# Kernel optimization log

Measured on AMD Instinct MI355X. Metric: run time of the kernel, lower is better.

Reference implementation:

```python
import jax, jax.numpy as jnp
import numpy as np
import math

EMBED_DIM = 128
SCALE = math.sqrt(EMBED_DIM)


def setup_inputs() -> dict:
    key = jax.random.key(0)
    # x: [B, N, D, L] = [4, 16, 128, 2048]
    x = jax.random.normal(key, (4, 16, 128, 2048), dtype=jnp.float32)
    return {"x": x}


def reference(x):
    # x: [B, N, D, L] -> [B, N, L, D]
    xt = jnp.swapaxes(x, -1, -2)
    # scores: [B, N, L, L] = softmax(x x^T / sqrt(D))
    scores = jnp.einsum("bnld,bnmd->bnlm", xt, xt) / jnp.asarray(SCALE, xt.dtype)
    attn = jax.nn.softmax(scores, axis=-1)
    # weighted values then mean over query positions L -> [B, N, D]
    out = jnp.einsum("bnlm,bnmd->bnld", attn, xt).mean(axis=2)
    return out
```

## Files before the change

kernel.cpp:

```cpp
#include <hip/hip_runtime.h>
#include <hip/hip_fp16.h>

#define H_  64
#define D_  128
#define L_  2048
#define PRE 0.35709578f
#define SLOTS 17

typedef _Float16 half8 __attribute__((ext_vector_type(8)));
typedef float    f32x4 __attribute__((ext_vector_type(4)));

__device__ __forceinline__ float fast_exp2(float x) {
#if __has_builtin(__builtin_amdgcn_exp2f)
    return __builtin_amdgcn_exp2f(x);
#else
    return __builtin_exp2f(x);
#endif
}

__device__ __forceinline__ void gload16(const void* g, void* l) {
    __builtin_amdgcn_global_load_lds(
        (const __attribute__((address_space(1))) void*)g,
        (__attribute__((address_space(3))) void*)l,
        16, 0, 0);
}

__device__ __forceinline__ void stage32k(const char* __restrict__ src,
                                         char* __restrict__ dst,
                                         int wid, int lane) {
#pragma unroll
    for (int jj = 0; jj < 8; ++jj) {
        const unsigned o   = (unsigned)(wid * 8 + jj) * 1024u + (unsigned)lane * 16u;
        const unsigned row = o >> 8;
        const unsigned so  = (o & ~255u) | ((o & 255u) ^ ((row & 7u) << 4));
        gload16(src + so, dst + (size_t)(wid * 8 + jj) * 1024u);
    }
}

__global__ __launch_bounds__(256) void k_transpose(const float* __restrict__ x,
                                                   __half* __restrict__ xt) {
    const int h  = blockIdx.x;
    const int lc = blockIdx.y;
    __shared__ float raw[128][65];
    const float* xh = x + (size_t)h * D_ * L_ + (size_t)lc * 64;
    const int t = threadIdx.x;
    const int r0 = t >> 4;
    const int c4 = (t & 15) << 2;
#pragma unroll
    for (int i = 0; i < 8; ++i) {
        const int d = i * 16 + r0;
        const float4 v = *(const float4*)(xh + (size_t)d * L_ + c4);
        raw[d][c4 + 0] = v.x; raw[d][c4 + 1] = v.y;
        raw[d][c4 + 2] = v.z; raw[d][c4 + 3] = v.w;
    }
    __syncthreads();
    const int lane = t & 63, w = t >> 6;
    __half2* xth = (__half2*)(xt + (size_t)h * L_ * D_ + (size_t)lc * 64 * D_);
#pragma unroll
    for (int i = 0; i < 16; ++i) {
        const int jl = w * 16 + i;
        const float a = raw[2 * lane][jl] * PRE;
        const float b = raw[2 * lane + 1][jl] * PRE;
        xth[(size_t)jl * 64 + lane] = __floats2half2_rn(a, b);
    }
}

template <int PASS>
__global__ __launch_bounds__(256, 2) void k_gemm(const __half* __restrict__ xt,
                                                 const float* __restrict__ ainv,
                                                 float* __restrict__ zw) {
    __shared__ char  sm[65536];
    __shared__ float aS[2048];
    __shared__ float csum[2][2][128];
    __shared__ float zfin[2][128];

    const int bid = blockIdx.x;
    const int res = bid & 7;
    const int j   = bid >> 3;
    const int h   = ((j >> 3) << 3) | res;
    const int pid = j & 7;

    const int t    = threadIdx.x;
    const int lane = t & 63;
    const int wid  = t >> 6;
    const int wr   = wid >> 1;
    const int wc   = wid & 1;
    const int lo   = lane & 15, hi = lane >> 4;
    const unsigned sx   = (unsigned)((lane & 7) << 4);
    const unsigned rowA = (unsigned)(wr * 64 + lo);
    const unsigned rowB = (unsigned)(wc * 64 + lo);

    const char* xh  = (const char*)(xt + (size_t)h * (L_ * D_));
    float*      zwh = zw + (size_t)h * SLOTS * 2048;

    if (PASS == 2) {
        const float4* a4 = (const float4*)(ainv + ((size_t)h << 11));
        *(float4*)&aS[t * 8]     = a4[t * 2];
        *(float4*)&aS[t * 8 + 4] = a4[t * 2 + 1];
    }

#pragma unroll 1
    for (int pp = 0; pp < 2; ++pp) {
        const int p  = pp ? (15 - pid) : pid;
        const int NS = 15 - p;

        stage32k(xh + (size_t)p * 32768, sm, wid, lane);
        if (NS > 0) stage32k(xh + (size_t)(p + 1) * 32768, sm + 32768, wid, lane);
        __syncthreads();

        half8 afr[4][4];
#pragma unroll
        for (int fm = 0; fm < 4; ++fm)
#pragma unroll
            for (int s = 0; s < 4; ++s)
                afr[fm][s] = *(const half8*)(sm + (rowA + fm * 16) * 256
                                                + (((unsigned)(s * 64 + hi * 16)) ^ sx));
        float rs[4][4] = {};
        float ar[4][4];
        if (PASS == 2) {
#pragma unroll
            for (int fm = 0; fm < 4; ++fm)
#pragma unroll
                for (int r = 0; r < 4; ++r)
                    ar[fm][r] = aS[p * 128 + wr * 64 + fm * 16 + hi * 4 + r];
        }

#pragma unroll 1
        for (int it = 0; it <= NS; ++it) {
            const int ct = p + it;
            if (it > 0) __syncthreads();
            if (it < NS)
                stage32k(xh + (size_t)(ct + 1) * 32768,
                         sm + (((it + 1) & 1) ? 32768 : 0), wid, lane);
            if (it >= 1 && t < 128) {
                const int pr = (it - 1) & 1;
                const float v = csum[pr][0][t] + csum[pr][1][t];
                if (it == 1) { if (PASS == 2) zwh[((size_t)16 << 11) + (size_t)p * 128 + t] = v; }
                else         zwh[((size_t)p << 11) + (size_t)(ct - 1) * 128 + t] = v;
            }

            const char* bbuf = (it == 0) ? sm : (sm + ((it & 1) ? 32768 : 0));

#pragma unroll 1
            for (int hf = 0; hf < 2; ++hf) {
                float acol[2];
                if (PASS == 2) {
#pragma unroll
                    for (int f = 0; f < 2; ++f)
                        acol[f] = aS[ct * 128 + wc * 64 + (hf * 2 + f) * 16 + lo];
                }
                f32x4 acc[4][2] = {};
                __builtin_amdgcn_s_setprio(1);
#pragma unroll
                for (int s = 0; s < 4; ++s) {
                    const unsigned inr = ((unsigned)(s * 64 + hi * 16)) ^ sx;
                    half8 b[2];
#pragma unroll
                    for (int f = 0; f < 2; ++f)
                        b[f] = *(const half8*)(bbuf + (rowB + (unsigned)(hf * 2 + f) * 16) * 256 + inr);
#pragma unroll
                    for (int fm = 0; fm < 4; ++fm)
#pragma unroll
                        for (int fn = 0; fn < 2; ++fn)
                            acc[fm][fn] = __builtin_amdgcn_mfma_f32_16x16x32_f16(
                                afr[fm][s], b[fn], acc[fm][fn], 0, 0, 0);
                }
                __builtin_amdgcn_s_setprio(0);

                float cs[2] = {0.f, 0.f};
#pragma unroll
                for (int fm = 0; fm < 4; ++fm)
#pragma unroll
                    for (int fn = 0; fn < 2; ++fn)
#pragma unroll
                        for (int r = 0; r < 4; ++r) {
                            const float e = fast_exp2(acc[fm][fn][r]);
                            if (PASS == 1) { rs[fm][r] += e; cs[fn] += e; }
                            else           { cs[fn] += ar[fm][r] * e;
                                             if (it > 0) rs[fm][r] += acol[fn] * e; }
                        }
                if (!(PASS == 1 && it == 0)) {
#pragma unroll
                    for (int fn = 0; fn < 2; ++fn) {
                        cs[fn] += __shfl_xor(cs[fn], 16, 64);
                        cs[fn] += __shfl_xor(cs[fn], 32, 64);
                    }
                    if (lane < 16) {
#pragma unroll
                        for (int fn = 0; fn < 2; ++fn)
                            csum[it & 1][wr][wc * 64 + (hf * 2 + fn) * 16 + lane] = cs[fn];
                    }
                }
            }
        }

#pragma unroll
        for (int fm = 0; fm < 4; ++fm)
#pragma unroll
            for (int r = 0; r < 4; ++r) {
                float v = rs[fm][r];
                v += __shfl_xor(v, 1, 64);
                v += __shfl_xor(v, 2, 64);
                v += __shfl_xor(v, 4, 64);
                v += __shfl_xor(v, 8, 64);
                if (lo == 0) zfin[wc][wr * 64 + fm * 16 + hi * 4 + r] = v;
            }
        __syncthreads();
        if (t < 128) {
            zwh[((size_t)15 << 11) + ((size_t)p << 7) + t] = zfin[0][t] + zfin[1][t];
            const int pr = NS & 1;
            const float v = csum[pr][0][t] + csum[pr][1][t];
            if (NS == 0) { if (PASS == 2) zwh[((size_t)16 << 11) + (size_t)p * 128 + t] = v; }
            else         zwh[((size_t)p << 11) + (size_t)(p + NS) * 128 + t] = v;
        }
    }
}

__global__ __launch_bounds__(256) void k_reduceZ(const float* __restrict__ zp,
                                                 float* __restrict__ ainv) {
    const int i = blockIdx.x * 256 + threadIdx.x;
    const int h = i >> 11, l = i & 2047, q = l >> 7;
    const float* zh = zp + (size_t)h * SLOTS * 2048;
    float z = zh[((size_t)15 << 11) + l];
#pragma unroll
    for (int p = 0; p < 15; ++p)
        if (p < q) z += zh[((size_t)p << 11) + l];
    ainv[i] = 1.0f / z;
}

__global__ __launch_bounds__(256) void k_out(const float* __restrict__ x,
                                             const float* __restrict__ wp,
                                             float* __restrict__ out) {
    __shared__ float wl[L_];
    const int h = blockIdx.x >> 2, qb = blockIdx.x & 3;
    const int t = threadIdx.x, lane = t & 63, wid = t >> 6;
    const float* wh = wp + (size_t)h * SLOTS * 2048;
    for (int c = t; c < L_; c += 256) {
        const int q = c >> 7;
        float s = wh[((size_t)15 << 11) + c] + wh[((size_t)16 << 11) + c];
#pragma unroll
        for (int p = 0; p < 15; ++p)
            if (p < q) s += wh[((size_t)p << 11) + c];
        wl[c] = s;
    }
    __syncthreads();
#pragma unroll 1
    for (int it = 0; it < 8; ++it) {
        const int d = qb * 32 + wid * 8 + it;
        const float* xr = x + ((size_t)h * D_ + d) * L_;
        float s = 0.0f;
#pragma unroll
        for (int kk = 0; kk < 8; ++kk) {
            const int m = kk * 256 + lane * 4;
            const float4 xv = *(const float4*)(xr + m);
            const float4 wv = *(const float4*)(wl + m);
            s += xv.x * wv.x + xv.y * wv.y + xv.z * wv.z + xv.w * wv.w;
        }
#pragma unroll
        for (int dm = 1; dm < 64; dm <<= 1) s += __shfl_xor(s, dm, 64);
        if (lane == 0) out[(size_t)h * D_ + d] = s * (1.0f / (float)L_);
    }
}

extern "C" void kernel_launch(void* const* d_in, const int* in_sizes, int n_in,
                              void* d_out, int out_size, void* d_ws, size_t ws_size,
                              hipStream_t stream) {
    const float* x = (const float*)d_in[0];
    float* out = (float*)d_out;
    char* ws = (char*)d_ws;

    __half* xt  = (__half*)(ws);
    float* zwp  = (float*)(ws + 33554432);
    float* ainv = (float*)(ws + 33554432 + 8912896);

    k_transpose<<<dim3(H_, L_ / 64), 256, 0, stream>>>(x, xt);
    k_gemm<1><<<512, 256, 0, stream>>>(xt, ainv, zwp);
    k_reduceZ<<<(H_ * L_) / 256, 256, 0, stream>>>(zwp, ainv);
    k_gemm<2><<<512, 256, 0, stream>>>(xt, ainv, zwp);
    k_out<<<H_ * 4, 256, 0, stream>>>(x, zwp, out);
}
```

Baseline: 160.4 us.

## Split gemm work into one 128-row panel per block with 64-column B tiles

Each k_gemm block now handles a single 128-row query panel instead of a paired panel (p, 15-p), and streams 64-column key tiles through a 32 KB double buffer instead of 128-column tiles through 64 KB. The grid doubles to 1024 blocks and launch bounds allow 3 blocks per CU, aiming for more concurrent waves and better latency hiding. In exchange, blocks now carry unequal work (triangular schedule, no longer balanced by pairing), and there are more barriers per unit of MFMA work.

```diff
diff --git a/kernel.cpp b/kernel.cpp
--- a/kernel.cpp
+++ b/kernel.cpp
@@ -25,15 +25,15 @@
         16, 0, 0);
 }
 
-__device__ __forceinline__ void stage32k(const char* __restrict__ src,
+__device__ __forceinline__ void stage16k(const char* __restrict__ src,
                                          char* __restrict__ dst,
                                          int wid, int lane) {
 #pragma unroll
-    for (int jj = 0; jj < 8; ++jj) {
-        const unsigned o   = (unsigned)(wid * 8 + jj) * 1024u + (unsigned)lane * 16u;
+    for (int jj = 0; jj < 4; ++jj) {
+        const unsigned o   = (unsigned)(wid * 4 + jj) * 1024u + (unsigned)lane * 16u;
         const unsigned row = o >> 8;
         const unsigned so  = (o & ~255u) | ((o & 255u) ^ ((row & 7u) << 4));
-        gload16(src + so, dst + (size_t)(wid * 8 + jj) * 1024u);
+        gload16(src + so, dst + (size_t)(wid * 4 + jj) * 1024u);
     }
 }
 
@@ -66,19 +66,20 @@
 }
 
 template <int PASS>
-__global__ __launch_bounds__(256, 2) void k_gemm(const __half* __restrict__ xt,
+__global__ __launch_bounds__(256, 3) void k_gemm(const __half* __restrict__ xt,
                                                  const float* __restrict__ ainv,
                                                  float* __restrict__ zw) {
-    __shared__ char  sm[65536];
+    __shared__ char  sm[32768];
     __shared__ float aS[2048];
-    __shared__ float csum[2][2][128];
+    __shared__ float csum[2][2][64];
     __shared__ float zfin[2][128];
 
     const int bid = blockIdx.x;
     const int res = bid & 7;
     const int j   = bid >> 3;
-    const int h   = ((j >> 3) << 3) | res;
-    const int pid = j & 7;
+    const int h   = ((j >> 4) << 3) | res;
+    const int p   = j & 15;
+    const int NTOT = 32 - 2 * p;
 
     const int t    = threadIdx.x;
     const int lane = t & 63;
@@ -87,8 +88,7 @@
     const int wc   = wid & 1;
     const int lo   = lane & 15, hi = lane >> 4;
     const unsigned sx   = (unsigned)((lane & 7) << 4);
-    const unsigned rowA = (unsigned)(wr * 64 + lo);
-    const unsigned rowB = (unsigned)(wc * 64 + lo);
+    const unsigned rowB = (unsigned)(wc * 32 + lo);
 
     const char* xh  = (const char*)(xt + (size_t)h * (L_ * D_));
     float*      zwh = zw + (size_t)h * SLOTS * 2048;
@@ -99,120 +99,112 @@
         *(float4*)&aS[t * 8 + 4] = a4[t * 2 + 1];
     }
 
+    stage16k(xh + (size_t)(2 * p) * 16384, sm, wid, lane);
+    stage16k(xh + (size_t)(2 * p + 1) * 16384, sm + 16384, wid, lane);
+    __syncthreads();
+
+    half8 afr[4][4];
+#pragma unroll
+    for (int f = 0; f < 4; ++f)
+#pragma unroll
+        for (int s = 0; s < 4; ++s)
+            afr[f][s] = *(const half8*)(sm + wr * 16384 + (unsigned)(f * 16 + lo) * 256
+                                           + (((unsigned)(s * 64 + hi * 16)) ^ sx));
+    float rs[4][4] = {};
+    float ar[4][4];
+    if (PASS == 2) {
+#pragma unroll
+        for (int fm = 0; fm < 4; ++fm)
+#pragma unroll
+            for (int r = 0; r < 4; ++r)
+                ar[fm][r] = aS[p * 128 + wr * 64 + fm * 16 + hi * 4 + r];
+    }
+
 #pragma unroll 1
-    for (int pp = 0; pp < 2; ++pp) {
-        const int p  = pp ? (15 - pid) : pid;
-        const int NS = 15 - p;
-
-        stage32k(xh + (size_t)p * 32768, sm, wid, lane);
-        if (NS > 0) stage32k(xh + (size_t)(p + 1) * 32768, sm + 32768, wid, lane);
-        __syncthreads();
-
-        half8 afr[4][4];
+    for (int i = 0; i < NTOT; ++i) {
+        const int cc = 2 * p + i;
+        if (i > 0) __syncthreads();
+        if (i >= 1 && i + 1 < NTOT)
+            stage16k(xh + (size_t)(cc + 1) * 16384,
+                     sm + (((i + 1) & 1) ? 16384 : 0), wid, lane);
+        if (i >= 1 && t < 64) {
+            const int jj = i - 1, c2 = 2 * p + jj;
+            const float v = csum[jj & 1][0][t] + csum[jj & 1][1][t];
+            if (jj < 2) { if (PASS == 2) zwh[((size_t)16 << 11) + (size_t)c2 * 64 + t] = v; }
+            else        zwh[((size_t)p << 11) + (size_t)c2 * 64 + t] = v;
+        }
+
+        const char* bbuf = sm + ((i & 1) ? 16384 : 0);
+        float acol[2];
+        if (PASS == 2) {
+#pragma unroll
+            for (int f = 0; f < 2; ++f)
+                acol[f] = aS[cc * 64 + wc * 32 + f * 16 + lo];
+        }
+
+        f32x4 acc[4][2] = {};
+        __builtin_amdgcn_s_setprio(1);
+#pragma unroll
+        for (int s = 0; s < 4; ++s) {
+            const unsigned inr = ((unsigned)(s * 64 + hi * 16)) ^ sx;
+            half8 b[2];
+#pragma unroll
+            for (int f = 0; f < 2; ++f)
+                b[f] = *(const half8*)(bbuf + (rowB + (unsigned)f * 16) * 256 + inr);
+#pragma unroll
+            for (int fm = 0; fm < 4; ++fm)
+#pragma unroll
+                for (int fn = 0; fn < 2; ++fn)
+                    acc[fm][fn] = __builtin_amdgcn_mfma_f32_16x16x32_f16(
+                        afr[fm][s], b[fn], acc[fm][fn], 0, 0, 0);
+        }
+        __builtin_amdgcn_s_setprio(0);
+
+        float cs[2] = {0.f, 0.f};
 #pragma unroll
         for (int fm = 0; fm < 4; ++fm)
 #pragma unroll
-            for (int s = 0; s < 4; ++s)
-                afr[fm][s] = *(const half8*)(sm + (rowA + fm * 16) * 256
-                                                + (((unsigned)(s * 64 + hi * 16)) ^ sx));
-        float rs[4][4] = {};
-        float ar[4][4];
-        if (PASS == 2) {
-#pragma unroll
-            for (int fm = 0; fm < 4; ++fm)
-#pragma unroll
-                for (int r = 0; r < 4; ++r)
-                    ar[fm][r] = aS[p * 128 + wr * 64 + fm * 16 + hi * 4 + r];
-        }
-
-#pragma unroll 1
-        for (int it = 0; it <= NS; ++it) {
-            const int ct = p + it;
-            if (it > 0) __syncthreads();
-            if (it < NS)
-                stage32k(xh + (size_t)(ct + 1) * 32768,
-                         sm + (((it + 1) & 1) ? 32768 : 0), wid, lane);
-            if (it >= 1 && t < 128) {
-                const int pr = (it - 1) & 1;
-                const float v = csum[pr][0][t] + csum[pr][1][t];
-                if (it == 1) { if (PASS == 2) zwh[((size_t)16 << 11) + (size_t)p * 128 + t] = v; }
-                else         zwh[((size_t)p << 11) + (size_t)(ct - 1) * 128 + t] = v;
+            for (int fn = 0; fn < 2; ++fn)
+#pragma unroll
+                for (int r = 0; r < 4; ++r) {
+                    const float e = fast_exp2(acc[fm][fn][r]);
+                    if (PASS == 1) { rs[fm][r] += e; cs[fn] += e; }
+                    else           { cs[fn] += ar[fm][r] * e;
+                                     if (i >= 2) rs[fm][r] += acol[fn] * e; }
+                }
+        if (!(PASS == 1 && i < 2)) {
+#pragma unroll
+            for (int fn = 0; fn < 2; ++fn) {
+                cs[fn] += __shfl_xor(cs[fn], 16, 64);
+                cs[fn] += __shfl_xor(cs[fn], 32, 64);
             }
-
-            const char* bbuf = (it == 0) ? sm : (sm + ((it & 1) ? 32768 : 0));
-
-#pragma unroll 1
-            for (int hf = 0; hf < 2; ++hf) {
-                float acol[2];
-                if (PASS == 2) {
-#pragma unroll
-                    for (int f = 0; f < 2; ++f)
-                        acol[f] = aS[ct * 128 + wc * 64 + (hf * 2 + f) * 16 + lo];
-                }
-                f32x4 acc[4][2] = {};
-                __builtin_amdgcn_s_setprio(1);
-#pragma unroll
-                for (int s = 0; s < 4; ++s) {
-                    const unsigned inr = ((unsigned)(s * 64 + hi * 16)) ^ sx;
-                    half8 b[2];
-#pragma unroll
-                    for (int f = 0; f < 2; ++f)
-                        b[f] = *(const half8*)(bbuf + (rowB + (unsigned)(hf * 2 + f) * 16) * 256 + inr);
-#pragma unroll
-                    for (int fm = 0; fm < 4; ++fm)
-#pragma unroll
-                        for (int fn = 0; fn < 2; ++fn)
-                            acc[fm][fn] = __builtin_amdgcn_mfma_f32_16x16x32_f16(
-                                afr[fm][s], b[fn], acc[fm][fn], 0, 0, 0);
-                }
-                __builtin_amdgcn_s_setprio(0);
-
-                float cs[2] = {0.f, 0.f};
-#pragma unroll
-                for (int fm = 0; fm < 4; ++fm)
-#pragma unroll
-                    for (int fn = 0; fn < 2; ++fn)
-#pragma unroll
-                        for (int r = 0; r < 4; ++r) {
-                            const float e = fast_exp2(acc[fm][fn][r]);
-                            if (PASS == 1) { rs[fm][r] += e; cs[fn] += e; }
-                            else           { cs[fn] += ar[fm][r] * e;
-                                             if (it > 0) rs[fm][r] += acol[fn] * e; }
-                        }
-                if (!(PASS == 1 && it == 0)) {
-#pragma unroll
-                    for (int fn = 0; fn < 2; ++fn) {
-                        cs[fn] += __shfl_xor(cs[fn], 16, 64);
-                        cs[fn] += __shfl_xor(cs[fn], 32, 64);
-                    }
-                    if (lane < 16) {
-#pragma unroll
-                        for (int fn = 0; fn < 2; ++fn)
-                            csum[it & 1][wr][wc * 64 + (hf * 2 + fn) * 16 + lane] = cs[fn];
-                    }
-                }
+            if (lane < 16) {
+#pragma unroll
+                for (int fn = 0; fn < 2; ++fn)
+                    csum[i & 1][wr][wc * 32 + fn * 16 + lane] = cs[fn];
             }
         }
-
-#pragma unroll
-        for (int fm = 0; fm < 4; ++fm)
-#pragma unroll
-            for (int r = 0; r < 4; ++r) {
-                float v = rs[fm][r];
-                v += __shfl_xor(v, 1, 64);
-                v += __shfl_xor(v, 2, 64);
-                v += __shfl_xor(v, 4, 64);
-                v += __shfl_xor(v, 8, 64);
-                if (lo == 0) zfin[wc][wr * 64 + fm * 16 + hi * 4 + r] = v;
-            }
-        __syncthreads();
-        if (t < 128) {
-            zwh[((size_t)15 << 11) + ((size_t)p << 7) + t] = zfin[0][t] + zfin[1][t];
-            const int pr = NS & 1;
-            const float v = csum[pr][0][t] + csum[pr][1][t];
-            if (NS == 0) { if (PASS == 2) zwh[((size_t)16 << 11) + (size_t)p * 128 + t] = v; }
-            else         zwh[((size_t)p << 11) + (size_t)(p + NS) * 128 + t] = v;
-        }
+    }
+
+#pragma unroll
+    for (int fm = 0; fm < 4; ++fm)
+#pragma unroll
+        for (int r = 0; r < 4; ++r) {
+            float v = rs[fm][r];
+            v += __shfl_xor(v, 1, 64);
+            v += __shfl_xor(v, 2, 64);
+            v += __shfl_xor(v, 4, 64);
+            v += __shfl_xor(v, 8, 64);
+            if (lo == 0) zfin[wc][wr * 64 + fm * 16 + hi * 4 + r] = v;
+        }
+    __syncthreads();
+    if (t < 128)
+        zwh[((size_t)15 << 11) + ((size_t)p << 7) + t] = zfin[0][t] + zfin[1][t];
+    if (t < 64) {
+        const int jj = NTOT - 1, c2 = 2 * p + jj;
+        const float v = csum[jj & 1][0][t] + csum[jj & 1][1][t];
+        if (jj < 2) { if (PASS == 2) zwh[((size_t)16 << 11) + (size_t)c2 * 64 + t] = v; }
+        else        zwh[((size_t)p << 11) + (size_t)c2 * 64 + t] = v;
     }
 }
 
@@ -274,8 +266,8 @@
     float* ainv = (float*)(ws + 33554432 + 8912896);
 
     k_transpose<<<dim3(H_, L_ / 64), 256, 0, stream>>>(x, xt);
-    k_gemm<1><<<512, 256, 0, stream>>>(xt, ainv, zwp);
+    k_gemm<1><<<1024, 256, 0, stream>>>(xt, ainv, zwp);
     k_reduceZ<<<(H_ * L_) / 256, 256, 0, stream>>>(zwp, ainv);
-    k_gemm<2><<<512, 256, 0, stream>>>(xt, ainv, zwp);
+    k_gemm<2><<<1024, 256, 0, stream>>>(xt, ainv, zwp);
     k_out<<<H_ * 4, 256, 0, stream>>>(x, zwp, out);
 }
```

Measured after the change: 189.8 us. +18.3%, slower.
